# Kernel tuning notes

Measured on AMD Instinct MI355X. Metric: run time of the kernel, lower is better.

## Reference

```python
import jax, jax.numpy as jnp
import numpy as np

N_NODES = 50000
N_EDGES = 800000
IN_FEAT = 128
HIDDEN = 128
N_CLASSES = 32


def setup_inputs() -> dict:
    key = jax.random.key(0)
    ks = jax.random.split(key, 8)
    x = jax.random.normal(ks[0], (N_NODES, IN_FEAT), dtype=jnp.float32)
    edge_index = jax.random.randint(ks[1], (2, N_EDGES), 0, N_NODES, dtype=jnp.int64)
    def glorot(k, fan_in, fan_out):
        s = jnp.sqrt(2.0 / (fan_in + fan_out)).astype(jnp.float32)
        return jax.random.normal(k, (fan_in, fan_out), dtype=jnp.float32) * s
    W1 = glorot(ks[2], IN_FEAT, 2 * HIDDEN)
    b1 = jnp.zeros((2 * HIDDEN,), dtype=jnp.float32)
    W2 = glorot(ks[3], 2 * HIDDEN, HIDDEN)
    b2 = jnp.zeros((HIDDEN,), dtype=jnp.float32)
    W3 = glorot(ks[4], HIDDEN, N_CLASSES)
    b3 = jnp.zeros((N_CLASSES,), dtype=jnp.float32)
    return {"x": x, "edge_index": edge_index, "W1": W1, "b1": b1,
            "W2": W2, "b2": b2, "W3": W3, "b3": b3}


def _gcn_norm(edge_index, num_nodes):
    # PyG GCNConv default: add self-loops, symmetric normalization D^-1/2 (A+I) D^-1/2
    loops = jnp.arange(num_nodes, dtype=edge_index.dtype)
    src = jnp.concatenate([edge_index[0], loops])
    dst = jnp.concatenate([edge_index[1], loops])
    ones = jnp.ones_like(dst, dtype=jnp.float32)
    deg = jax.ops.segment_sum(ones, dst, num_segments=num_nodes)
    dinv = jnp.where(deg > 0, 1.0 / jnp.sqrt(deg), 0.0)
    norm = dinv[src] * dinv[dst]  # [E + N]
    return src, dst, norm


def _gcn_conv(x, src, dst, norm, W, b, num_nodes):
    h = x @ W                               # [N, out]
    msg = h[src] * norm[:, None]            # gather + per-edge scale, [E+N, out]
    agg = jax.ops.segment_sum(msg, dst, num_segments=num_nodes)  # scatter-add
    return agg + b


def reference(x, edge_index, W1, b1, W2, b2, W3, b3):
    n = x.shape[0]
    src, dst, norm = _gcn_norm(edge_index, n)
    h = jax.nn.relu(_gcn_conv(x, src, dst, norm, W1, b1, n))
    h = jax.nn.relu(_gcn_conv(h, src, dst, norm, W2, b2, n))
    return _gcn_conv(h, src, dst, norm, W3, b3, n)
```

## Files before the change

### kernel.cpp

```cpp
#include <hip/hip_runtime.h>
#include <hip/hip_fp16.h>

#define NN 50000
#define NE 800000
#define NBKT 391
#define P1B 128

typedef __attribute__((ext_vector_type(8))) _Float16 half8v;
typedef __attribute__((ext_vector_type(4))) float f32x4;

static inline size_t align_up(size_t x, size_t a) { return (x + a - 1) & ~(a - 1); }

union U8 {
    ushort4 u;
    __half2 h[2];
};

__device__ __forceinline__ float4 u8_to_f4(ushort4 uu) {
    U8 c;
    c.u = uu;
    float2 f01 = __half22float2(c.h[0]);
    float2 f23 = __half22float2(c.h[1]);
    return make_float4(f01.x, f01.y, f23.x, f23.y);
}

__device__ __forceinline__ ushort4 f4_to_u8(float4 v) {
    U8 c;
    c.h[0] = __floats2half2_rn(v.x, v.y);
    c.h[1] = __floats2half2_rn(v.z, v.w);
    return c.u;
}

__device__ __forceinline__ int detect64(const int* __restrict__ e) {
    int ok = 1;
    for (int k = 1; k < 64; k += 2) ok &= (e[k] == 0);
    return ok;
}

__global__ __launch_bounds__(256) void bucket_hist(const int* __restrict__ e,
                                                   int* __restrict__ gcount,
                                                   int* __restrict__ base, int E) {
    __shared__ int hist[NBKT];
    const int is64 = detect64(e);
    for (int t = threadIdx.x; t < NBKT; t += 256) hist[t] = 0;
    __syncthreads();
    const int chunk = (E + P1B - 1) / P1B;
    const int b0 = blockIdx.x * chunk;
    const int b1 = min(E, b0 + chunk);
    for (int i = b0 + threadIdx.x; i < b1; i += 256) {
        int d = is64 ? e[2 * (E + i)] : e[E + i];
        atomicAdd(&hist[d >> 7], 1);
    }
    __syncthreads();
    for (int t = threadIdx.x; t < NBKT; t += 256)
        base[blockIdx.x * NBKT + t] = atomicAdd(&gcount[t], hist[t]);
}

__global__ __launch_bounds__(512) void bucket_scan(const int* __restrict__ gcount,
                                                   int* __restrict__ bstart, int nb) {
    __shared__ int s[512];
    const int t = threadIdx.x;
    int v = (t < nb) ? gcount[t] : 0;
    s[t] = v;
    __syncthreads();
    for (int off = 1; off < 512; off <<= 1) {
        int tv = (t >= off) ? s[t - off] : 0;
        __syncthreads();
        s[t] += tv;
        __syncthreads();
    }
    if (t < nb) bstart[t] = s[t] - v;
    if (t == 0) bstart[nb] = s[511];
}

__global__ __launch_bounds__(256) void bucket_scatter(const int* __restrict__ e,
                                                      const int* __restrict__ bstart,
                                                      const int* __restrict__ base,
                                                      int2* __restrict__ pairs, int E) {
    __shared__ int cur[NBKT];
    const int is64 = detect64(e);
    for (int t = threadIdx.x; t < NBKT; t += 256)
        cur[t] = bstart[t] + base[blockIdx.x * NBKT + t];
    __syncthreads();
    const int chunk = (E + P1B - 1) / P1B;
    const int b0 = blockIdx.x * chunk;
    const int b1 = min(E, b0 + chunk);
    for (int i = b0 + threadIdx.x; i < b1; i += 256) {
        int s = is64 ? e[2 * i] : e[i];
        int d = is64 ? e[2 * (E + i)] : e[E + i];
        int pos = atomicAdd(&cur[d >> 7], 1);
        pairs[pos] = make_int2(s, d);
    }
}

__global__ __launch_bounds__(256) void bucket_finalize(const int2* __restrict__ pairs,
                                                       const int* __restrict__ bstart,
                                                       int* __restrict__ row_start,
                                                       int* __restrict__ deg_cnt,
                                                       float* __restrict__ dinv,
                                                       int* __restrict__ csr, int n) {
    __shared__ int ldeg[128];
    __shared__ int lscan[128];
    __shared__ int cur[128];
    const int bkt = blockIdx.x;
    const int s0 = bstart[bkt], s1 = bstart[bkt + 1];
    if (threadIdx.x < 128) ldeg[threadIdx.x] = 0;
    __syncthreads();
    for (int i = s0 + threadIdx.x; i < s1; i += 256)
        atomicAdd(&ldeg[pairs[i].y & 127], 1);
    __syncthreads();
    if (threadIdx.x < 128) lscan[threadIdx.x] = ldeg[threadIdx.x];
    __syncthreads();
    for (int off = 1; off < 128; off <<= 1) {
        int v = 0;
        if (threadIdx.x < 128 && threadIdx.x >= off) v = lscan[threadIdx.x - off];
        __syncthreads();
        if (threadIdx.x < 128) lscan[threadIdx.x] += v;
        __syncthreads();
    }
    if (threadIdx.x < 128) {
        int node = (bkt << 7) + threadIdx.x;
        int exc = s0 + lscan[threadIdx.x] - ldeg[threadIdx.x];
        cur[threadIdx.x] = exc;
        if (node < n) {
            row_start[node] = exc;
            deg_cnt[node] = ldeg[threadIdx.x];
            dinv[node] = rsqrtf((float)(ldeg[threadIdx.x] + 1));
        }
    }
    __syncthreads();
    for (int i = s0 + threadIdx.x; i < s1; i += 256) {
        int2 pr = pairs[i];
        int pos = atomicAdd(&cur[pr.y & 127], 1);
        csr[pos] = pr.x;
    }
}

__global__ void prep_weights_all(const float* __restrict__ W1, const float* __restrict__ W2,
                                 const float* __restrict__ W3,
                                 unsigned short* __restrict__ w1th, unsigned short* __restrict__ w1tl,
                                 unsigned short* __restrict__ w2th, unsigned short* __restrict__ w2tl,
                                 unsigned short* __restrict__ w3th, unsigned short* __restrict__ w3tl,
                                 int* __restrict__ gcount) {
    int i = blockIdx.x * blockDim.x + threadIdx.x;
    if (i < NBKT + 1) gcount[i] = 0;
    const float* W;
    unsigned short *th, *tl;
    int K, M, j;
    if (i < 32768)      { W = W1; th = w1th; tl = w1tl; K = 128; M = 256; j = i; }
    else if (i < 65536) { W = W2; th = w2th; tl = w2tl; K = 256; M = 128; j = i - 32768; }
    else if (i < 69632) { W = W3; th = w3th; tl = w3tl; K = 128; M = 32;  j = i - 65536; }
    else return;
    int k = j / M, m = j % M;
    float v = W[j];
    __half h = __float2half_rn(v);
    __half l = __float2half_rn(v - __half2float(h));
    th[(size_t)m * K + k] = __half_as_ushort(h);
    tl[(size_t)m * K + k] = __half_as_ushort(l);
}

template <int L>
__global__ void cast_f16_scaled(const float* __restrict__ in, const float* __restrict__ dinv,
                                unsigned short* __restrict__ out, int total4) {
    int i = blockIdx.x * blockDim.x + threadIdx.x;
    if (i >= total4) return;
    float4 v = ((const float4*)in)[i];
    float s = dinv[i / L];
    v.x *= s; v.y *= s; v.z *= s; v.w *= s;
    ((ushort4*)out)[i] = f4_to_u8(v);
}

template <int BM, int BN, int WM, int WN, bool BIAS, bool RELU, bool OUTF16, bool SCALE>
__global__ __launch_bounds__(256) void gemm_f16(
    const unsigned short* __restrict__ A,
    const unsigned short* __restrict__ Wth, const unsigned short* __restrict__ Wtl,
    const float* __restrict__ bias, const float* __restrict__ dscale,
    float* __restrict__ Cf, unsigned short* __restrict__ Ch,
    int N, int K, int M) {
    constexpr int KS = 32;
    constexpr int LDA = KS + 8;
    constexpr int WTM = BM / WM;
    constexpr int WTN = BN / WN;
    constexpr int FM = WTM / 16;
    constexpr int FN = WTN / 16;
    __shared__ unsigned short sA[BM][LDA], sWh[BN][LDA], sWl[BN][LDA];

    const int tid = threadIdx.x;
    const int lane = tid & 63;
    const int w = tid >> 6;
    const int wr = w / WN, wc = w % WN;
    const int row0 = blockIdx.y * BM;
    const int col0 = blockIdx.x * BN;

    f32x4 acc[FM][FN];
#pragma unroll
    for (int m = 0; m < FM; ++m)
#pragma unroll
        for (int nn = 0; nn < FN; ++nn) {
            f32x4 z = {0.f, 0.f, 0.f, 0.f};
            acc[m][nn] = z;
        }

    for (int k0 = 0; k0 < K; k0 += KS) {
        for (int idx = tid; idx < BM * KS / 8; idx += 256) {
            int r = idx / (KS / 8);
            int s = idx % (KS / 8);
            int gr = row0 + r;
            int4 va = make_int4(0, 0, 0, 0);
            if (gr < N) va = *(const int4*)&A[(size_t)gr * K + k0 + s * 8];
            *(int4*)&sA[r][s * 8] = va;
        }
        for (int idx = tid; idx < BN * KS / 8; idx += 256) {
            int c = idx / (KS / 8);
            int s = idx % (KS / 8);
            int gc = col0 + c;
            *(int4*)&sWh[c][s * 8] = *(const int4*)&Wth[(size_t)gc * K + k0 + s * 8];
            *(int4*)&sWl[c][s * 8] = *(const int4*)&Wtl[(size_t)gc * K + k0 + s * 8];
        }
        __syncthreads();

        half8v af[FM], wfh[FN], wfl[FN];
        const int koff = (lane >> 4) * 8;
        const int rsel = lane & 15;
#pragma unroll
        for (int m = 0; m < FM; ++m)
            af[m] = *(const half8v*)&sA[wr * WTM + m * 16 + rsel][koff];
#pragma unroll
        for (int nn = 0; nn < FN; ++nn) {
            wfh[nn] = *(const half8v*)&sWh[wc * WTN + nn * 16 + rsel][koff];
            wfl[nn] = *(const half8v*)&sWl[wc * WTN + nn * 16 + rsel][koff];
        }
#pragma unroll
        for (int m = 0; m < FM; ++m)
#pragma unroll
            for (int nn = 0; nn < FN; ++nn) {
                acc[m][nn] = __builtin_amdgcn_mfma_f32_16x16x32_f16(af[m], wfh[nn], acc[m][nn], 0, 0, 0);
                acc[m][nn] = __builtin_amdgcn_mfma_f32_16x16x32_f16(af[m], wfl[nn], acc[m][nn], 0, 0, 0);
            }
        __syncthreads();
    }

#pragma unroll
    for (int m = 0; m < FM; ++m) {
#pragma unroll
        for (int r = 0; r < 4; ++r) {
            int row = row0 + wr * WTM + m * 16 + (lane >> 4) * 4 + r;
            if (row >= N) continue;
            float rs = SCALE ? dscale[row] : 1.f;
#pragma unroll
            for (int nn = 0; nn < FN; ++nn) {
                int col = col0 + wc * WTN + nn * 16 + (lane & 15);
                float v = acc[m][nn][r];
                if (BIAS) v += bias[col];
                if (RELU) v = fmaxf(v, 0.f);
                if (SCALE) v *= rs;
                if constexpr (OUTF16) {
                    Ch[(size_t)row * M + col] = __half_as_ushort(__float2half_rn(v));
                } else {
                    Cf[(size_t)row * M + col] = v;
                }
            }
        }
    }
}

__device__ __forceinline__ float4 add4(float4 v, float4 a) {
    a.x += v.x; a.y += v.y; a.z += v.z; a.w += v.w;
    return a;
}

template <int F, int NPB, bool BIAS, bool RELU, bool OUTF16>
__global__ __launch_bounds__((F / 4) * NPB) void agg4h(
    const unsigned short* __restrict__ h, const int* __restrict__ row_start,
    const int* __restrict__ deg_cnt, const int* __restrict__ csr,
    const float* __restrict__ dinv, const float* __restrict__ bias,
    float* __restrict__ outf, unsigned short* __restrict__ outh, int n) {
    constexpr int L = F / 4;
    const int local = threadIdx.x / L;
    const int lane = threadIdx.x % L;
    const int node = blockIdx.x * NPB + local;
    if (node >= n) return;

    const ushort4* __restrict__ h4 = (const ushort4*)h;
    const float di = dinv[node];

    float4 acc = u8_to_f4(h4[(size_t)node * L + lane]);

    const int beg = row_start[node];
    const int num = deg_cnt[node];
    int e = 0;
    for (; e + 8 <= num; e += 8) {
        int c[8];
        float4 v[8];
#pragma unroll
        for (int u = 0; u < 8; ++u) c[u] = csr[beg + e + u];
#pragma unroll
        for (int u = 0; u < 8; ++u) v[u] = u8_to_f4(h4[(size_t)c[u] * L + lane]);
#pragma unroll
        for (int u = 0; u < 8; ++u) acc = add4(v[u], acc);
    }
    for (; e < num; ++e) {
        const int c = csr[beg + e];
        acc = add4(u8_to_f4(h4[(size_t)c * L + lane]), acc);
    }
    acc.x *= di; acc.y *= di; acc.z *= di; acc.w *= di;
    if (BIAS) {
        const float4 b = ((const float4*)bias)[lane];
        acc.x += b.x; acc.y += b.y; acc.z += b.z; acc.w += b.w;
    }
    if (RELU) {
        acc.x = fmaxf(acc.x, 0.f); acc.y = fmaxf(acc.y, 0.f);
        acc.z = fmaxf(acc.z, 0.f); acc.w = fmaxf(acc.w, 0.f);
    }
    if constexpr (OUTF16) {
        ((ushort4*)outh)[(size_t)node * L + lane] = f4_to_u8(acc);
    } else {
        ((float4*)outf)[(size_t)node * L + lane] = acc;
    }
}

extern "C" void kernel_launch(void* const* d_in, const int* in_sizes, int n_in,
                              void* d_out, int out_size, void* d_ws, size_t ws_size,
                              hipStream_t stream) {
    const float* x   = (const float*)d_in[0];
    const int*   eix = (const int*)d_in[1];
    const float* W1  = (const float*)d_in[2];
    const float* b1  = (const float*)d_in[3];
    const float* W2  = (const float*)d_in[4];
    const float* b2  = (const float*)d_in[5];
    const float* W3  = (const float*)d_in[6];
    const float* b3  = (const float*)d_in[7];
    float* out = (float*)d_out;

    const int n = NN, E = NE;

    char* p = (char*)d_ws;
    auto alloc = [&](size_t bytes) { void* r = (void*)p; p += align_up(bytes, 256); return r; };
    int*   deg_cnt   = (int*)alloc((size_t)n * 4);
    float* dinv      = (float*)alloc((size_t)n * 4);
    int*   row_start = (int*)alloc((size_t)n * 4);
    int*   gcount    = (int*)alloc((size_t)(NBKT + 1) * 4);
    int*   bstart    = (int*)alloc((size_t)(NBKT + 1) * 4);
    int*   base      = (int*)alloc((size_t)P1B * NBKT * 4);
    int2*  pairs     = (int2*)alloc((size_t)E * 8);
    int*   csr       = (int*)alloc((size_t)E * 4);
    unsigned short* w1th = (unsigned short*)alloc((size_t)128 * 256 * 2);
    unsigned short* w1tl = (unsigned short*)alloc((size_t)128 * 256 * 2);
    unsigned short* w2th = (unsigned short*)alloc((size_t)256 * 128 * 2);
    unsigned short* w2tl = (unsigned short*)alloc((size_t)256 * 128 * 2);
    unsigned short* w3th = (unsigned short*)alloc((size_t)128 * 32 * 2);
    unsigned short* w3tl = (unsigned short*)alloc((size_t)128 * 32 * 2);
    unsigned short* xh    = (unsigned short*)alloc((size_t)n * 128 * 2);
    unsigned short* agg0  = (unsigned short*)alloc((size_t)n * 128 * 2);
    unsigned short* h1    = (unsigned short*)alloc((size_t)n * 256 * 2);
    unsigned short* h2s   = (unsigned short*)alloc((size_t)n * 128 * 2);
    unsigned short* x3    = (unsigned short*)alloc((size_t)n * 128 * 2);
    unsigned short* h3s   = (unsigned short*)alloc((size_t)n * 32 * 2);
    (void)ws_size; (void)in_sizes; (void)n_in; (void)out_size;

    prep_weights_all<<<(69632 + 255) / 256, 256, 0, stream>>>(
        W1, W2, W3, w1th, w1tl, w2th, w2tl, w3th, w3tl, gcount);

    bucket_hist<<<P1B, 256, 0, stream>>>(eix, gcount, base, E);
    bucket_scan<<<1, 512, 0, stream>>>(gcount, bstart, NBKT);
    bucket_scatter<<<P1B, 256, 0, stream>>>(eix, bstart, base, pairs, E);
    bucket_finalize<<<NBKT, 256, 0, stream>>>(pairs, bstart, row_start, deg_cnt, dinv, csr, n);

    cast_f16_scaled<32><<<((n * 128 / 4) + 255) / 256, 256, 0, stream>>>(
        x, dinv, xh, n * 128 / 4);

    const int RB = (n + 127) / 128;

    agg4h<128, 8, false, false, true><<<(n + 7) / 8, 256, 0, stream>>>(
        xh, row_start, deg_cnt, csr, dinv, nullptr, nullptr, agg0, n);
    gemm_f16<128, 128, 2, 2, true, true, true, false><<<dim3(2, RB), 256, 0, stream>>>(
        agg0, w1th, w1tl, b1, nullptr, nullptr, h1, n, 128, 256);

    gemm_f16<128, 128, 2, 2, false, false, true, true><<<dim3(1, RB), 256, 0, stream>>>(
        h1, w2th, w2tl, nullptr, dinv, nullptr, h2s, n, 256, 128);
    agg4h<128, 8, true, true, true><<<(n + 7) / 8, 256, 0, stream>>>(
        h2s, row_start, deg_cnt, csr, dinv, b2, nullptr, x3, n);

    gemm_f16<128, 32, 4, 1, false, false, true, true><<<dim3(1, RB), 256, 0, stream>>>(
        x3, w3th, w3tl, nullptr, dinv, nullptr, h3s, n, 128, 32);
    agg4h<32, 32, true, false, false><<<(n + 31) / 32, 256, 0, stream>>>(
        h3s, row_start, deg_cnt, csr, dinv, b3, out, nullptr, n);
}
```

Measured before the change: 183.8 us.

## Compress edge indices to 16-bit, fuse x cast, drop split-fp16 weights

```diff
diff --git a/kernel.cpp b/kernel.cpp
--- a/kernel.cpp
+++ b/kernel.cpp
@@ -76,7 +76,7 @@
 __global__ __launch_bounds__(256) void bucket_scatter(const int* __restrict__ e,
                                                       const int* __restrict__ bstart,
                                                       const int* __restrict__ base,
-                                                      int2* __restrict__ pairs, int E) {
+                                                      unsigned* __restrict__ pairs, int E) {
     __shared__ int cur[NBKT];
     const int is64 = detect64(e);
     for (int t = threadIdx.x; t < NBKT; t += 256)
@@ -89,25 +89,28 @@
         int s = is64 ? e[2 * i] : e[i];
         int d = is64 ? e[2 * (E + i)] : e[E + i];
         int pos = atomicAdd(&cur[d >> 7], 1);
-        pairs[pos] = make_int2(s, d);
-    }
-}
-
-__global__ __launch_bounds__(256) void bucket_finalize(const int2* __restrict__ pairs,
+        pairs[pos] = (unsigned)s | ((unsigned)(d & 127) << 16);
+    }
+}
+
+__global__ __launch_bounds__(256) void bucket_finalize(const unsigned* __restrict__ pairs,
                                                        const int* __restrict__ bstart,
+                                                       const float* __restrict__ x,
                                                        int* __restrict__ row_start,
                                                        int* __restrict__ deg_cnt,
                                                        float* __restrict__ dinv,
-                                                       int* __restrict__ csr, int n) {
+                                                       unsigned short* __restrict__ csr,
+                                                       unsigned short* __restrict__ xh, int n) {
     __shared__ int ldeg[128];
     __shared__ int lscan[128];
     __shared__ int cur[128];
+    __shared__ float sdinv[128];
     const int bkt = blockIdx.x;
     const int s0 = bstart[bkt], s1 = bstart[bkt + 1];
     if (threadIdx.x < 128) ldeg[threadIdx.x] = 0;
     __syncthreads();
     for (int i = s0 + threadIdx.x; i < s1; i += 256)
-        atomicAdd(&ldeg[pairs[i].y & 127], 1);
+        atomicAdd(&ldeg[pairs[i] >> 16], 1);
     __syncthreads();
     if (threadIdx.x < 128) lscan[threadIdx.x] = ldeg[threadIdx.x];
     __syncthreads();
@@ -122,58 +125,56 @@
         int node = (bkt << 7) + threadIdx.x;
         int exc = s0 + lscan[threadIdx.x] - ldeg[threadIdx.x];
         cur[threadIdx.x] = exc;
+        float di = rsqrtf((float)(ldeg[threadIdx.x] + 1));
+        sdinv[threadIdx.x] = di;
         if (node < n) {
             row_start[node] = exc;
             deg_cnt[node] = ldeg[threadIdx.x];
-            dinv[node] = rsqrtf((float)(ldeg[threadIdx.x] + 1));
+            dinv[node] = di;
         }
     }
     __syncthreads();
     for (int i = s0 + threadIdx.x; i < s1; i += 256) {
-        int2 pr = pairs[i];
-        int pos = atomicAdd(&cur[pr.y & 127], 1);
-        csr[pos] = pr.x;
+        unsigned pr = pairs[i];
+        int pos = atomicAdd(&cur[pr >> 16], 1);
+        csr[pos] = (unsigned short)(pr & 0xFFFFu);
+    }
+    for (int idx = threadIdx.x; idx < 128 * 32; idx += 256) {
+        int ln = idx >> 5;
+        int c4 = idx & 31;
+        int node = (bkt << 7) + ln;
+        if (node < n) {
+            float4 v = ((const float4*)x)[(size_t)node * 32 + c4];
+            float s = sdinv[ln];
+            v.x *= s; v.y *= s; v.z *= s; v.w *= s;
+            ((ushort4*)xh)[(size_t)node * 32 + c4] = f4_to_u8(v);
+        }
     }
 }
 
 __global__ void prep_weights_all(const float* __restrict__ W1, const float* __restrict__ W2,
                                  const float* __restrict__ W3,
-                                 unsigned short* __restrict__ w1th, unsigned short* __restrict__ w1tl,
-                                 unsigned short* __restrict__ w2th, unsigned short* __restrict__ w2tl,
-                                 unsigned short* __restrict__ w3th, unsigned short* __restrict__ w3tl,
+                                 unsigned short* __restrict__ w1t,
+                                 unsigned short* __restrict__ w2t,
+                                 unsigned short* __restrict__ w3t,
                                  int* __restrict__ gcount) {
     int i = blockIdx.x * blockDim.x + threadIdx.x;
     if (i < NBKT + 1) gcount[i] = 0;
     const float* W;
-    unsigned short *th, *tl;
+    unsigned short* th;
     int K, M, j;
-    if (i < 32768)      { W = W1; th = w1th; tl = w1tl; K = 128; M = 256; j = i; }
-    else if (i < 65536) { W = W2; th = w2th; tl = w2tl; K = 256; M = 128; j = i - 32768; }
-    else if (i < 69632) { W = W3; th = w3th; tl = w3tl; K = 128; M = 32;  j = i - 65536; }
+    if (i < 32768)      { W = W1; th = w1t; K = 128; M = 256; j = i; }
+    else if (i < 65536) { W = W2; th = w2t; K = 256; M = 128; j = i - 32768; }
+    else if (i < 69632) { W = W3; th = w3t; K = 128; M = 32;  j = i - 65536; }
     else return;
     int k = j / M, m = j % M;
-    float v = W[j];
-    __half h = __float2half_rn(v);
-    __half l = __float2half_rn(v - __half2float(h));
-    th[(size_t)m * K + k] = __half_as_ushort(h);
-    tl[(size_t)m * K + k] = __half_as_ushort(l);
-}
-
-template <int L>
-__global__ void cast_f16_scaled(const float* __restrict__ in, const float* __restrict__ dinv,
-                                unsigned short* __restrict__ out, int total4) {
-    int i = blockIdx.x * blockDim.x + threadIdx.x;
-    if (i >= total4) return;
-    float4 v = ((const float4*)in)[i];
-    float s = dinv[i / L];
-    v.x *= s; v.y *= s; v.z *= s; v.w *= s;
-    ((ushort4*)out)[i] = f4_to_u8(v);
+    th[(size_t)m * K + k] = __half_as_ushort(__float2half_rn(W[j]));
 }
 
 template <int BM, int BN, int WM, int WN, bool BIAS, bool RELU, bool OUTF16, bool SCALE>
 __global__ __launch_bounds__(256) void gemm_f16(
     const unsigned short* __restrict__ A,
-    const unsigned short* __restrict__ Wth, const unsigned short* __restrict__ Wtl,
+    const unsigned short* __restrict__ Wt,
     const float* __restrict__ bias, const float* __restrict__ dscale,
     float* __restrict__ Cf, unsigned short* __restrict__ Ch,
     int N, int K, int M) {
@@ -183,7 +184,7 @@
     constexpr int WTN = BN / WN;
     constexpr int FM = WTM / 16;
     constexpr int FN = WTN / 16;
-    __shared__ unsigned short sA[BM][LDA], sWh[BN][LDA], sWl[BN][LDA];
+    __shared__ unsigned short sA[BM][LDA], sW[BN][LDA];
 
     const int tid = threadIdx.x;
     const int lane = tid & 63;
@@ -214,29 +215,24 @@
             int c = idx / (KS / 8);
             int s = idx % (KS / 8);
             int gc = col0 + c;
-            *(int4*)&sWh[c][s * 8] = *(const int4*)&Wth[(size_t)gc * K + k0 + s * 8];
-            *(int4*)&sWl[c][s * 8] = *(const int4*)&Wtl[(size_t)gc * K + k0 + s * 8];
-        }
-        __syncthreads();
-
-        half8v af[FM], wfh[FN], wfl[FN];
+            *(int4*)&sW[c][s * 8] = *(const int4*)&Wt[(size_t)gc * K + k0 + s * 8];
+        }
+        __syncthreads();
+
+        half8v af[FM], wf[FN];
         const int koff = (lane >> 4) * 8;
         const int rsel = lane & 15;
 #pragma unroll
         for (int m = 0; m < FM; ++m)
             af[m] = *(const half8v*)&sA[wr * WTM + m * 16 + rsel][koff];
 #pragma unroll
-        for (int nn = 0; nn < FN; ++nn) {
-            wfh[nn] = *(const half8v*)&sWh[wc * WTN + nn * 16 + rsel][koff];
-            wfl[nn] = *(const half8v*)&sWl[wc * WTN + nn * 16 + rsel][koff];
-        }
+        for (int nn = 0; nn < FN; ++nn)
+            wf[nn] = *(const half8v*)&sW[wc * WTN + nn * 16 + rsel][koff];
 #pragma unroll
         for (int m = 0; m < FM; ++m)
 #pragma unroll
-            for (int nn = 0; nn < FN; ++nn) {
-                acc[m][nn] = __builtin_amdgcn_mfma_f32_16x16x32_f16(af[m], wfh[nn], acc[m][nn], 0, 0, 0);
-                acc[m][nn] = __builtin_amdgcn_mfma_f32_16x16x32_f16(af[m], wfl[nn], acc[m][nn], 0, 0, 0);
-            }
+            for (int nn = 0; nn < FN; ++nn)
+                acc[m][nn] = __builtin_amdgcn_mfma_f32_16x16x32_f16(af[m], wf[nn], acc[m][nn], 0, 0, 0);
         __syncthreads();
     }
 
@@ -272,7 +268,7 @@
 template <int F, int NPB, bool BIAS, bool RELU, bool OUTF16>
 __global__ __launch_bounds__((F / 4) * NPB) void agg4h(
     const unsigned short* __restrict__ h, const int* __restrict__ row_start,
-    const int* __restrict__ deg_cnt, const int* __restrict__ csr,
+    const int* __restrict__ deg_cnt, const unsigned short* __restrict__ csr,
     const float* __restrict__ dinv, const float* __restrict__ bias,
     float* __restrict__ outf, unsigned short* __restrict__ outh, int n) {
     constexpr int L = F / 4;
@@ -291,13 +287,13 @@
     int e = 0;
     for (; e + 8 <= num; e += 8) {
         int c[8];
-        float4 v[8];
+        ushort4 raw[8];
 #pragma unroll
         for (int u = 0; u < 8; ++u) c[u] = csr[beg + e + u];
 #pragma unroll
-        for (int u = 0; u < 8; ++u) v[u] = u8_to_f4(h4[(size_t)c[u] * L + lane]);
-#pragma unroll
-        for (int u = 0; u < 8; ++u) acc = add4(v[u], acc);
+        for (int u = 0; u < 8; ++u) raw[u] = h4[(size_t)c[u] * L + lane];
+#pragma unroll
+        for (int u = 0; u < 8; ++u) acc = add4(u8_to_f4(raw[u]), acc);
     }
     for (; e < num; ++e) {
         const int c = csr[beg + e];
@@ -342,47 +338,42 @@
     int*   gcount    = (int*)alloc((size_t)(NBKT + 1) * 4);
     int*   bstart    = (int*)alloc((size_t)(NBKT + 1) * 4);
     int*   base      = (int*)alloc((size_t)P1B * NBKT * 4);
-    int2*  pairs     = (int2*)alloc((size_t)E * 8);
-    int*   csr       = (int*)alloc((size_t)E * 4);
-    unsigned short* w1th = (unsigned short*)alloc((size_t)128 * 256 * 2);
-    unsigned short* w1tl = (unsigned short*)alloc((size_t)128 * 256 * 2);
-    unsigned short* w2th = (unsigned short*)alloc((size_t)256 * 128 * 2);
-    unsigned short* w2tl = (unsigned short*)alloc((size_t)256 * 128 * 2);
-    unsigned short* w3th = (unsigned short*)alloc((size_t)128 * 32 * 2);
-    unsigned short* w3tl = (unsigned short*)alloc((size_t)128 * 32 * 2);
-    unsigned short* xh    = (unsigned short*)alloc((size_t)n * 128 * 2);
-    unsigned short* agg0  = (unsigned short*)alloc((size_t)n * 128 * 2);
-    unsigned short* h1    = (unsigned short*)alloc((size_t)n * 256 * 2);
-    unsigned short* h2s   = (unsigned short*)alloc((size_t)n * 128 * 2);
-    unsigned short* x3    = (unsigned short*)alloc((size_t)n * 128 * 2);
-    unsigned short* h3s   = (unsigned short*)alloc((size_t)n * 32 * 2);
+    unsigned* pairs  = (unsigned*)alloc((size_t)E * 4);
+    unsigned short* csr = (unsigned short*)alloc((size_t)E * 2);
+    unsigned short* w1t = (unsigned short*)alloc((size_t)128 * 256 * 2);
+    unsigned short* w2t = (unsigned short*)alloc((size_t)256 * 128 * 2);
+    unsigned short* w3t = (unsigned short*)alloc((size_t)128 * 32 * 2);
+    unsigned short* xh   = (unsigned short*)alloc((size_t)n * 128 * 2);
+    unsigned short* agg0 = (unsigned short*)alloc((size_t)n * 128 * 2);
+    unsigned short* h1   = (unsigned short*)alloc((size_t)n * 256 * 2);
+    unsigned short* h2s  = (unsigned short*)alloc((size_t)n * 128 * 2);
+    unsigned short* x3   = (unsigned short*)alloc((size_t)n * 128 * 2);
+    unsigned short* h3s  = (unsigned short*)alloc((size_t)n * 32 * 2);
     (void)ws_size; (void)in_sizes; (void)n_in; (void)out_size;
 
     prep_weights_all<<<(69632 + 255) / 256, 256, 0, stream>>>(
-        W1, W2, W3, w1th, w1tl, w2th, w2tl, w3th, w3tl, gcount);
+        W1, W2, W3, w1t, w2t, w3t, gcount);
 
     bucket_hist<<<P1B, 256, 0, stream>>>(eix, gcount, base, E);
     bucket_scan<<<1, 512, 0, stream>>>(gcount, bstart, NBKT);
     bucket_scatter<<<P1B, 256, 0, stream>>>(eix, bstart, base, pairs, E);
-    bucket_finalize<<<NBKT, 256, 0, stream>>>(pairs, bstart, row_start, deg_cnt, dinv, csr, n);
-
-    cast_f16_scaled<32><<<((n * 128 / 4) + 255) / 256, 256, 0, stream>>>(
-        x, dinv, xh, n * 128 / 4);
+    bucket_finalize<<<NBKT, 256, 0, stream>>>(pairs, bstart, x, row_start, deg_cnt,
+                                              dinv, csr, xh, n);
 
     const int RB = (n + 127) / 128;
 
     agg4h<128, 8, false, false, true><<<(n + 7) / 8, 256, 0, stream>>>(
         xh, row_start, deg_cnt, csr, dinv, nullptr, nullptr, agg0, n);
     gemm_f16<128, 128, 2, 2, true, true, true, false><<<dim3(2, RB), 256, 0, stream>>>(
-        agg0, w1th, w1tl, b1, nullptr, nullptr, h1, n, 128, 256);
+        agg0, w1t, b1, nullptr, nullptr, h1, n, 128, 256);
 
     gemm_f16<128, 128, 2, 2, false, false, true, true><<<dim3(1, RB), 256, 0, stream>>>(
-        h1, w2th, w2tl, nullptr, dinv, nullptr, h2s, n, 256, 128);
+        h1, w2t, nullptr, dinv, nullptr, h2s, n, 256, 128);
     agg4h<128, 8, true, true, true><<<(n + 7) / 8, 256, 0, stream>>>(
         h2s, row_start, deg_cnt, csr, dinv, b2, nullptr, x3, n);
 
     gemm_f16<128, 32, 4, 1, false, false, true, true><<<dim3(1, RB), 256, 0, stream>>>(
-        x3, w3th, w3tl, nullptr, dinv, nullptr, h3s, n, 128, 32);
+        x3, w3t, nullptr, dinv, nullptr, h3s, n, 128, 32);
     agg4h<32, 32, true, false, false><<<(n + 31) / 32, 256, 0, stream>>>(
         h3s, row_start, deg_cnt, csr, dinv, b3, out, nullptr, n);
 }
```

Result: faster. 177.0 us (-3.7%).
